# Kernel tuning notes

Measured on AMD Instinct MI355X. Metric: run time of the kernel, lower is better.

Reference implementation:

```python
import jax, jax.numpy as jnp
import numpy as np

N, H, HD = 512, 8, 128          # n_nodes, n_heads, h feature dim
M0, M1 = 256, 256               # mlp_units
NORM_CONST = 1.0


def setup_inputs() -> dict:
    key = jax.random.key(0)
    ks = jax.random.split(key, 16)
    def w(k, i, o, scale=1.0):
        return jax.random.normal(k, (i, o), jnp.float32) * (scale / np.sqrt(i))
    F = HD + H * H               # h_concat dim = 128 + 64 = 192
    EIN = H + 2 * F              # edge MLP input dim = 8 + 384 = 392
    return {
        "x": jax.random.normal(ks[0], (N, H, 3), jnp.float32),
        "h": jax.random.normal(ks[1], (N, HD), jnp.float32),
        # phi_e: MLP([256,256], silu, activate_final=True)
        "We0": w(ks[2], EIN, M0), "be0": jnp.zeros((M0,), jnp.float32),
        "We1": w(ks[3], M0, M1), "be1": jnp.zeros((M1,), jnp.float32),
        # phi_inf: Linear(1) + sigmoid
        "Winf": w(ks[4], M1, 1), "binf": jnp.zeros((1,), jnp.float32),
        # phi_x: MLP([256,256], silu, activate_final=True) -> Linear(n_heads) (variance-scaled small init)
        "Wx0": w(ks[5], M1, M0), "bx0": jnp.zeros((M0,), jnp.float32),
        "Wx1": w(ks[6], M0, M1), "bx1": jnp.zeros((M1,), jnp.float32),
        "Wxo": w(ks[7], M1, H, scale=0.03), "bxo": jnp.zeros((H,), jnp.float32),
        # phi_h: MLP([256,256], silu, activate_final=False)... note haiku MLP applies
        # activation between layers; final Linear(h_dim) appended in forward.
        "Wh0": w(ks[8], M1 + HD, M0), "bh0": jnp.zeros((M0,), jnp.float32),
        "Wh1": w(ks[9], M0, M1), "bh1": jnp.zeros((M1,), jnp.float32),
        "Who": w(ks[10], M1, HD), "bho": jnp.zeros((HD,), jnp.float32),
    }


def _forward(x, h, We0, be0, We1, be1, Winf, binf, Wx0, bx0, Wx1, bx1,
             Wxo, bxo, Wh0, bh0, Wh1, bh1, Who, bho):
    n, nh = x.shape[0], x.shape[1]
    silu = jax.nn.silu
    off = 1.0 - jnp.eye(n, dtype=x.dtype)                  # off-diagonal node mask
    # per-node head-pair squared distances -> [N, H*H] (diag naturally 0)
    dh = x[:, :, None, :] - x[:, None, :, :]               # [N,H,H,3]
    sqh = jnp.sum(dh * dh, axis=-1).reshape(n, nh * nh)
    hc = jnp.concatenate([h, sqh], axis=-1)                # [N, F]
    # all-pairs node diffs per head: dn[i,j,h] = x[j,h] - x[i,h]
    dn = x[None] - x[:, None]                              # [N,N,H,3]
    sqn = jnp.sum(dn * dn, axis=-1)                        # [N,N,H]
    F = hc.shape[-1]
    hc_j = jnp.broadcast_to(hc[None], (n, n, F))           # receiver-side: hc[j]
    hc_i = jnp.broadcast_to(hc[:, None], (n, n, F))        # sender-side: hc[i]
    edge_in = jnp.concatenate([sqn, hc_j, hc_i], axis=-1)  # [N,N,H+2F]
    # phi_e (activate_final=True), zero self-edges
    m = silu(silu(edge_in @ We0 + be0) @ We1 + be1) * off[:, :, None]
    # gate + message aggregation
    e = jax.nn.sigmoid(m @ Winf + binf)[..., 0] * off      # [N,N]
    m_i = jnp.einsum('ijd,ij->id', m, e)                   # [N,M1]
    # phi_x multi-head coordinate weights (tanh=False), zero self-edges
    px = (silu(silu(m @ Wx0 + bx0) @ Wx1 + bx1) @ Wxo + bxo) * off[:, :, None]
    # normalize_by_x_norm=True path
    norm = jnp.sqrt(sqn + 1e-8) + NORM_CONST               # [N,N,H]
    ndiff = (dn / norm[..., None]) * off[:, :, None, None]
    shift = jnp.einsum('ijhd,ijh->ihd', ndiff, px) / (n - 1)  # agg='mean'
    x_new = x + shift
    # phi_h with residual
    ph_in = jnp.concatenate([m_i, h], axis=-1)
    h_new = h + silu(silu(ph_in @ Wh0 + bh0) @ Wh1 + bh1) @ Who + bho
    return x_new, h_new


def reference(x, h, We0, be0, We1, be1, Winf, binf, Wx0, bx0, Wx1, bx1,
              Wxo, bxo, Wh0, bh0, Wh1, bh1, Who, bho):
    return _forward(x, h, We0, be0, We1, be1, Winf, binf, Wx0, bx0, Wx1, bx1,
                    Wxo, bxo, Wh0, bh0, Wh1, bh1, Who, bho)
```

## Files before the change

### kernel.cpp

```cpp
#include <hip/hip_runtime.h>
#include <math.h>

#define N_NODES 512
#define NH 8
#define HD 128
#define M 256
#define PITCH 264
#define JTILE 64
#define RPW 16

typedef __bf16 v8bf __attribute__((ext_vector_type(8)));
typedef float f32x4 __attribute__((ext_vector_type(4)));
typedef unsigned short us4v __attribute__((ext_vector_type(4)));

__device__ __forceinline__ float silu_f(float v) {
  return v * __builtin_amdgcn_rcpf(1.f + __expf(-v));
}
__device__ __forceinline__ float sigmoid_f(float v) {
  return __builtin_amdgcn_rcpf(1.f + __expf(-v));
}
__device__ __forceinline__ unsigned short f2bf(float f) {
  unsigned u = __float_as_uint(f);
  u += 0x7fffu + ((u >> 16) & 1u);
  return (unsigned short)(u >> 16);
}
__device__ __forceinline__ unsigned short f2bf_hi(float f) {
  return (unsigned short)((__float_as_uint(f) + 0x8000u) >> 16);
}
__device__ __forceinline__ float bf2f(unsigned short s) {
  return __uint_as_float(((unsigned)s) << 16);
}

__device__ __forceinline__ void gl2lds16(const unsigned short* g, unsigned short* l) {
  __builtin_amdgcn_global_load_lds(
      (const __attribute__((address_space(1))) unsigned int*)g,
      (__attribute__((address_space(3))) unsigned int*)l, 16, 0, 0);
}

__global__ __launch_bounds__(256) void k_pre(
    const float* __restrict__ x, const float* __restrict__ h,
    const float* __restrict__ We0, const float* __restrict__ be0,
    const float* __restrict__ We1, const float* __restrict__ Wx0,
    const float* __restrict__ Wx1, const float* __restrict__ Wxo,
    unsigned short* __restrict__ wsB,
    float* __restrict__ P, float* __restrict__ Q,
    float* __restrict__ mi, float* __restrict__ shift)
{
  const int t = threadIdx.x;
  if (blockIdx.x < 816) {
    const int gid = blockIdx.x * 256 + t;
    if (gid >= 208896) return;
    float val;
    if (gid < 196608) {
      const int layer = gid >> 16;
      const int i2 = gid & 65535;
      const int j = i2 & 7, lane = (i2 >> 3) & 63, nt = (i2 >> 9) & 15, kt = i2 >> 13;
      const int k = kt * 32 + (lane >> 4) * 8 + j;
      const int n = nt * 16 + (lane & 15);
      const float* W = (layer == 0) ? We1 : (layer == 1) ? Wx0 : Wx1;
      val = W[k * 256 + n];
    } else if (gid < 200704) {
      const int i2 = gid - 196608;
      const int j = i2 & 7, lane = (i2 >> 3) & 63, kt = (i2 >> 9) & 7;
      const int k = kt * 32 + (lane >> 4) * 8 + j;
      const int n = lane & 15;
      val = (n < 8) ? Wxo[k * 8 + n] : 0.f;
    } else {
      const int i2 = gid - 200704;
      const int j = i2 & 7, lane = (i2 >> 3) & 63, nt = i2 >> 9;
      const int quad = lane >> 4, lnib = lane & 15;
      val = (quad == 0) ? We0[j * 256 + nt * 16 + lnib] : 0.f;
    }
    wsB[gid] = f2bf(val);
    return;
  }
  const int i = blockIdx.x - 816;
  __shared__ float s_x[24];
  __shared__ float s_hc[192];
  mi[i * M + t] = 0.f;
  if (t < 24) { shift[i * 24 + t] = 0.f; s_x[t] = x[i * 24 + t]; }
  __syncthreads();
  if (t < HD) {
    s_hc[t] = h[i * HD + t];
  } else if (t < 192) {
    const int p = t - HD, a = p >> 3, b = p & 7;
    float s = 0.f;
#pragma unroll
    for (int d = 0; d < 3; ++d) {
      const float dx = s_x[a * 3 + d] - s_x[b * 3 + d];
      s = fmaf(dx, dx, s);
    }
    s_hc[t] = s;
  }
  __syncthreads();
  float p = 0.f, q = 0.f;
  for (int k = 0; k < 192; ++k) {
    const float hv = s_hc[k];
    p = fmaf(hv, We0[(8 + k) * M + t], p);
    q = fmaf(hv, We0[(200 + k) * M + t], q);
  }
  P[i * M + t] = p;
  Q[i * M + t] = q + be0[t];
}

__global__ __launch_bounds__(256, 3) void k_edge(
    const float* __restrict__ x,
    const float* __restrict__ P, const float* __restrict__ Q,
    const float* __restrict__ be1,
    const float* __restrict__ Winf, const float* __restrict__ binf,
    const float* __restrict__ bx0, const float* __restrict__ bx1,
    const float* __restrict__ bxo,
    const unsigned short* __restrict__ wsB,
    float* __restrict__ mi_acc, float* __restrict__ shift_acc)
{
  const int i  = blockIdx.x;
  const int j0 = blockIdx.y * JTILE;
  const int t  = threadIdx.x;
  const int lane = t & 63, wave = t >> 6;
  const int lnib = lane & 15, quad = lane >> 4;
  const int r0 = wave * RPW;
  const int jw = j0 + r0;

  __shared__ __align__(16) unsigned short a_act[JTILE * PITCH];
  __shared__ __align__(16) unsigned short B_buf[8192];
  __shared__ __align__(16) float s_sqn[JTILE][8];
  __shared__ __align__(16) unsigned short s_sqnb[JTILE][8];
  __shared__ float s_e[JTILE];

#pragma unroll
  for (int kk = 0; kk < 2; ++kk) {
    const int idx = kk * 64 + lane;
    const int r = idx >> 3, hh = idx & 7;
    const int j = jw + r;
    float s = 0.f;
#pragma unroll
    for (int d = 0; d < 3; ++d) {
      const float dx = x[j * 24 + hh * 3 + d] - x[i * 24 + hh * 3 + d];
      s = fmaf(dx, dx, s);
    }
    s_sqn[r0 + r][hh] = s;
    s_sqnb[r0 + r][hh] = f2bf(s);
  }

  const float binf0 = binf[0];

  f32x4 acc[16];

  {
#pragma unroll
    for (int nt = 0; nt < 16; ++nt)
#pragma unroll
      for (int reg = 0; reg < 4; ++reg)
        acc[nt][reg] = P[(jw + quad * 4 + reg) * M + nt * 16 + lnib];
    const v8bf aS = *(const v8bf*)&s_sqnb[r0 + lnib][0];
    const unsigned short* B0 = wsB + 200704;
#pragma unroll
    for (int nt = 0; nt < 16; ++nt) {
      const v8bf bv = *(const v8bf*)&B0[(nt * 64 + lane) * 8];
      acc[nt] = __builtin_amdgcn_mfma_f32_16x16x32_bf16(aS, bv, acc[nt], 0, 0, 0);
    }
#pragma unroll
    for (int nt = 0; nt < 16; ++nt) {
      const float qv = Q[i * M + nt * 16 + lnib];
#pragma unroll
      for (int reg = 0; reg < 4; ++reg) {
        const int row = r0 + quad * 4 + reg;
        a_act[row * PITCH + nt * 16 + lnib] = f2bf_hi(silu_f(acc[nt][reg] + qv));
      }
    }
  }

  auto run_gemm = [&](const unsigned short* __restrict__ Bg) {
#pragma unroll
    for (int kt = 0; kt < 8; ++kt) {
      __syncthreads();
      {
        const unsigned short* src = Bg + kt * 8192 + wave * 2048 + lane * 8;
        unsigned short* dst = &B_buf[wave * 2048];
        gl2lds16(src,        dst);
        gl2lds16(src + 512,  dst + 512);
        gl2lds16(src + 1024, dst + 1024);
        gl2lds16(src + 1536, dst + 1536);
      }
      __syncthreads();
      const v8bf a0 = *(const v8bf*)&a_act[(r0 + lnib) * PITCH + kt * 32 + quad * 8];
#pragma unroll
      for (int nt = 0; nt < 16; ++nt) {
        const v8bf bv = *(const v8bf*)&B_buf[nt * 512 + lane * 8];
        acc[nt] = __builtin_amdgcn_mfma_f32_16x16x32_bf16(a0, bv, acc[nt], 0, 0, 0);
      }
    }
  };

#pragma unroll
  for (int nt = 0; nt < 16; ++nt) {
    const float b = be1[nt * 16 + lnib];
    acc[nt] = (f32x4){b, b, b, b};
  }
  run_gemm(wsB);
  {
    float ge[4] = {0.f, 0.f, 0.f, 0.f};
#pragma unroll
    for (int nt = 0; nt < 16; ++nt) {
      const float wfv = Winf[nt * 16 + lnib];
#pragma unroll
      for (int reg = 0; reg < 4; ++reg) {
        float v = silu_f(acc[nt][reg]);
        const int row = r0 + quad * 4 + reg;
        if (j0 + row == i) v = 0.f;
        a_act[row * PITCH + nt * 16 + lnib] = f2bf_hi(v);
        ge[reg] = fmaf(v, wfv, ge[reg]);
      }
    }
#pragma unroll
    for (int reg = 0; reg < 4; ++reg) {
      float g = ge[reg];
      g += __shfl_xor(g, 1);
      g += __shfl_xor(g, 2);
      g += __shfl_xor(g, 4);
      g += __shfl_xor(g, 8);
      const float ev = sigmoid_f(g + binf0);
      if (lnib == 0) s_e[r0 + quad * 4 + reg] = ev;
    }
  }

  {
    const int c0 = lane * 4;
    f32x4 mip = (f32x4){0.f, 0.f, 0.f, 0.f};
#pragma unroll
    for (int r = 0; r < RPW; ++r) {
      const us4v mv = *(const us4v*)&a_act[(r0 + r) * PITCH + c0];
      const float ev = s_e[r0 + r];
      mip[0] = fmaf(bf2f(mv[0]), ev, mip[0]);
      mip[1] = fmaf(bf2f(mv[1]), ev, mip[1]);
      mip[2] = fmaf(bf2f(mv[2]), ev, mip[2]);
      mip[3] = fmaf(bf2f(mv[3]), ev, mip[3]);
    }
    atomicAdd(&mi_acc[i * M + c0 + 0], mip[0]);
    atomicAdd(&mi_acc[i * M + c0 + 1], mip[1]);
    atomicAdd(&mi_acc[i * M + c0 + 2], mip[2]);
    atomicAdd(&mi_acc[i * M + c0 + 3], mip[3]);
  }

#pragma unroll
  for (int nt = 0; nt < 16; ++nt) {
    const float b = bx0[nt * 16 + lnib];
    acc[nt] = (f32x4){b, b, b, b};
  }
  run_gemm(wsB + 65536);
#pragma unroll
  for (int nt = 0; nt < 16; ++nt)
#pragma unroll
    for (int reg = 0; reg < 4; ++reg) {
      const int row = r0 + quad * 4 + reg;
      a_act[row * PITCH + nt * 16 + lnib] = f2bf_hi(silu_f(acc[nt][reg]));
    }

#pragma unroll
  for (int nt = 0; nt < 16; ++nt) {
    const float b = bx1[nt * 16 + lnib];
    acc[nt] = (f32x4){b, b, b, b};
  }
  run_gemm(wsB + 131072);
#pragma unroll
  for (int nt = 0; nt < 16; ++nt)
#pragma unroll
    for (int reg = 0; reg < 4; ++reg) {
      const int row = r0 + quad * 4 + reg;
      a_act[row * PITCH + nt * 16 + lnib] = f2bf_hi(silu_f(acc[nt][reg]));
    }

  f32x4 px;
  {
    const float b = (lnib < 8) ? bxo[lnib] : 0.f;
    px = (f32x4){b, b, b, b};
    const unsigned short* B = wsB + 196608;
#pragma unroll
    for (int kt = 0; kt < 8; ++kt) {
      const v8bf a0 = *(const v8bf*)&a_act[(r0 + lnib) * PITCH + kt * 32 + quad * 8];
      const v8bf bv = *(const v8bf*)&B[(kt * 64 + lane) * 8];
      px = __builtin_amdgcn_mfma_f32_16x16x32_bf16(a0, bv, px, 0, 0, 0);
    }
  }

  {
    const int hh = lnib & 7;
    const float xi0 = x[i * 24 + hh * 3 + 0];
    const float xi1 = x[i * 24 + hh * 3 + 1];
    const float xi2 = x[i * 24 + hh * 3 + 2];
    float p0 = 0.f, p1 = 0.f, p2 = 0.f;
#pragma unroll
    for (int reg = 0; reg < 4; ++reg) {
      const int row = r0 + quad * 4 + reg;
      const int jg = j0 + row;
      if (jg != i) {
        const float pxv = px[reg];
        const float sq  = s_sqn[row][hh];
        const float f   = pxv * __builtin_amdgcn_rcpf(sqrtf(sq + 1e-8f) + 1.f);
        p0 = fmaf(x[jg * 24 + hh * 3 + 0] - xi0, f, p0);
        p1 = fmaf(x[jg * 24 + hh * 3 + 1] - xi1, f, p1);
        p2 = fmaf(x[jg * 24 + hh * 3 + 2] - xi2, f, p2);
      }
    }
    p0 += __shfl_xor(p0, 16); p0 += __shfl_xor(p0, 32);
    p1 += __shfl_xor(p1, 16); p1 += __shfl_xor(p1, 32);
    p2 += __shfl_xor(p2, 16); p2 += __shfl_xor(p2, 32);
    if (lane < 8) {
      atomicAdd(&shift_acc[i * 24 + hh * 3 + 0], p0);
      atomicAdd(&shift_acc[i * 24 + hh * 3 + 1], p1);
      atomicAdd(&shift_acc[i * 24 + hh * 3 + 2], p2);
    }
  }
}

__global__ __launch_bounds__(256) void k_hout(
    const float* __restrict__ x, const float* __restrict__ shift,
    const float* __restrict__ h, const float* __restrict__ mi,
    const float* __restrict__ Wh0, const float* __restrict__ bh0,
    const float* __restrict__ Wh1, const float* __restrict__ bh1,
    const float* __restrict__ Who, const float* __restrict__ bho,
    float* __restrict__ out_x, float* __restrict__ out_h)
{
  const int i = blockIdx.x, t = threadIdx.x;
  __shared__ float s_in[M + HD];
  __shared__ float s_b[M];
  if (t < 24) out_x[i * 24 + t] = x[i * 24 + t] + shift[i * 24 + t] * (1.f / 511.f);
  s_in[t] = mi[i * M + t];
  if (t < HD) s_in[M + t] = h[i * HD + t];
  __syncthreads();
  float acc = bh0[t];
  for (int k = 0; k < M + HD; ++k) acc = fmaf(s_in[k], Wh0[k * M + t], acc);
  s_b[t] = silu_f(acc);
  __syncthreads();
  float acc2 = bh1[t];
  for (int k = 0; k < M; ++k) acc2 = fmaf(s_b[k], Wh1[k * M + t], acc2);
  const float a1v = silu_f(acc2);
  __syncthreads();
  s_in[t] = a1v;
  __syncthreads();
  if (t < HD) {
    float o = bho[t];
    for (int k = 0; k < M; ++k) o = fmaf(s_in[k], Who[k * HD + t], o);
    out_h[i * HD + t] = h[i * HD + t] + o;
  }
}

extern "C" void kernel_launch(void* const* d_in, const int* in_sizes, int n_in,
                              void* d_out, int out_size, void* d_ws, size_t ws_size,
                              hipStream_t stream)
{
  const float* x    = (const float*)d_in[0];
  const float* h    = (const float*)d_in[1];
  const float* We0  = (const float*)d_in[2];
  const float* be0  = (const float*)d_in[3];
  const float* We1  = (const float*)d_in[4];
  const float* be1  = (const float*)d_in[5];
  const float* Winf = (const float*)d_in[6];
  const float* binf = (const float*)d_in[7];
  const float* Wx0  = (const float*)d_in[8];
  const float* bx0  = (const float*)d_in[9];
  const float* Wx1  = (const float*)d_in[10];
  const float* bx1  = (const float*)d_in[11];
  const float* Wxo  = (const float*)d_in[12];
  const float* bxo  = (const float*)d_in[13];
  const float* Wh0  = (const float*)d_in[14];
  const float* bh0  = (const float*)d_in[15];
  const float* Wh1  = (const float*)d_in[16];
  const float* bh1  = (const float*)d_in[17];
  const float* Who  = (const float*)d_in[18];
  const float* bho  = (const float*)d_in[19];

  float* out_x = (float*)d_out;
  float* out_h = out_x + N_NODES * NH * 3;

  float* ws    = (float*)d_ws;
  float* mi    = ws;
  float* shift = ws + 131072;
  float* P     = ws + 143360;
  float* Q     = ws + 274432;
  unsigned short* wsB = (unsigned short*)(ws + 405504);

  k_pre<<<816 + N_NODES, 256, 0, stream>>>(
      x, h, We0, be0, We1, Wx0, Wx1, Wxo, wsB, P, Q, mi, shift);
  k_edge<<<dim3(N_NODES, N_NODES / JTILE), 256, 0, stream>>>(
      x, P, Q, be1, Winf, binf, bx0, bx1, bxo, wsB, mi, shift);
  k_hout<<<N_NODES, 256, 0, stream>>>(
      x, shift, h, mi, Wh0, bh0, Wh1, bh1, Who, bho, out_x, out_h);
}
```

Measured before the change: 316.8 us.

## Split edge-kernel output columns across two waves per row group with 512 threads

The edge kernel now launches 512 threads, and each pair of waves shares a 16-row group, each wave owning half of the 256 output columns. This halves the per-wave accumulator registers and splits B-tile staging across eight waves, aiming for more resident waves and better latency hiding. In exchange it needs extra barriers: one after each GEMM, plus a shared-memory cross-wave reduction for the gate logit. The final px projection runs on only half the waves.

Measured after the change: 321.6 us. No clear change (+1.5%).

```diff
diff --git a/kernel.cpp b/kernel.cpp
--- a/kernel.cpp
+++ b/kernel.cpp
@@ -103,7 +103,7 @@
   Q[i * M + t] = q + be0[t];
 }
 
-__global__ __launch_bounds__(256, 3) void k_edge(
+__global__ __launch_bounds__(512, 4) void k_edge(
     const float* __restrict__ x,
     const float* __restrict__ P, const float* __restrict__ Q,
     const float* __restrict__ be1,
@@ -118,14 +118,24 @@
   const int t  = threadIdx.x;
   const int lane = t & 63, wave = t >> 6;
   const int lnib = lane & 15, quad = lane >> 4;
-  const int r0 = wave * RPW;
+  const int rg = wave >> 1, c = wave & 1;
+  const int r0 = rg * RPW;
   const int jw = j0 + r0;
+  const int cb = c * 128;
 
   __shared__ __align__(16) unsigned short a_act[JTILE * PITCH];
   __shared__ __align__(16) unsigned short B_buf[8192];
   __shared__ __align__(16) float s_sqn[JTILE][8];
   __shared__ __align__(16) unsigned short s_sqnb[JTILE][8];
+  __shared__ float s_red[JTILE][2];
   __shared__ float s_e[JTILE];
+
+  auto stage = [&](const unsigned short* __restrict__ Bg, int kt) {
+    const unsigned short* src = Bg + kt * 8192 + wave * 1024 + lane * 8;
+    unsigned short* dst = &B_buf[wave * 1024];
+    gl2lds16(src,       dst);
+    gl2lds16(src + 512, dst + 512);
+  };
 
 #pragma unroll
   for (int kk = 0; kk < 2; ++kk) {
@@ -144,28 +154,28 @@
 
   const float binf0 = binf[0];
 
-  f32x4 acc[16];
+  f32x4 acc[8];
 
   {
 #pragma unroll
-    for (int nt = 0; nt < 16; ++nt)
+    for (int nt = 0; nt < 8; ++nt)
 #pragma unroll
       for (int reg = 0; reg < 4; ++reg)
-        acc[nt][reg] = P[(jw + quad * 4 + reg) * M + nt * 16 + lnib];
+        acc[nt][reg] = P[(jw + quad * 4 + reg) * M + cb + nt * 16 + lnib];
     const v8bf aS = *(const v8bf*)&s_sqnb[r0 + lnib][0];
     const unsigned short* B0 = wsB + 200704;
 #pragma unroll
-    for (int nt = 0; nt < 16; ++nt) {
-      const v8bf bv = *(const v8bf*)&B0[(nt * 64 + lane) * 8];
+    for (int nt = 0; nt < 8; ++nt) {
+      const v8bf bv = *(const v8bf*)&B0[((c * 8 + nt) * 64 + lane) * 8];
       acc[nt] = __builtin_amdgcn_mfma_f32_16x16x32_bf16(aS, bv, acc[nt], 0, 0, 0);
     }
 #pragma unroll
-    for (int nt = 0; nt < 16; ++nt) {
-      const float qv = Q[i * M + nt * 16 + lnib];
+    for (int nt = 0; nt < 8; ++nt) {
+      const float qv = Q[i * M + cb + nt * 16 + lnib];
 #pragma unroll
       for (int reg = 0; reg < 4; ++reg) {
         const int row = r0 + quad * 4 + reg;
-        a_act[row * PITCH + nt * 16 + lnib] = f2bf_hi(silu_f(acc[nt][reg] + qv));
+        a_act[row * PITCH + cb + nt * 16 + lnib] = f2bf_hi(silu_f(acc[nt][reg] + qv));
       }
     }
   }
@@ -174,41 +184,35 @@
 #pragma unroll
     for (int kt = 0; kt < 8; ++kt) {
       __syncthreads();
-      {
-        const unsigned short* src = Bg + kt * 8192 + wave * 2048 + lane * 8;
-        unsigned short* dst = &B_buf[wave * 2048];
-        gl2lds16(src,        dst);
-        gl2lds16(src + 512,  dst + 512);
-        gl2lds16(src + 1024, dst + 1024);
-        gl2lds16(src + 1536, dst + 1536);
-      }
+      stage(Bg, kt);
       __syncthreads();
       const v8bf a0 = *(const v8bf*)&a_act[(r0 + lnib) * PITCH + kt * 32 + quad * 8];
 #pragma unroll
-      for (int nt = 0; nt < 16; ++nt) {
-        const v8bf bv = *(const v8bf*)&B_buf[nt * 512 + lane * 8];
+      for (int nt = 0; nt < 8; ++nt) {
+        const v8bf bv = *(const v8bf*)&B_buf[(c * 8 + nt) * 512 + lane * 8];
         acc[nt] = __builtin_amdgcn_mfma_f32_16x16x32_bf16(a0, bv, acc[nt], 0, 0, 0);
       }
     }
+    __syncthreads();
   };
 
 #pragma unroll
-  for (int nt = 0; nt < 16; ++nt) {
-    const float b = be1[nt * 16 + lnib];
+  for (int nt = 0; nt < 8; ++nt) {
+    const float b = be1[cb + nt * 16 + lnib];
     acc[nt] = (f32x4){b, b, b, b};
   }
   run_gemm(wsB);
   {
     float ge[4] = {0.f, 0.f, 0.f, 0.f};
 #pragma unroll
-    for (int nt = 0; nt < 16; ++nt) {
-      const float wfv = Winf[nt * 16 + lnib];
+    for (int nt = 0; nt < 8; ++nt) {
+      const float wfv = Winf[cb + nt * 16 + lnib];
 #pragma unroll
       for (int reg = 0; reg < 4; ++reg) {
         float v = silu_f(acc[nt][reg]);
         const int row = r0 + quad * 4 + reg;
         if (j0 + row == i) v = 0.f;
-        a_act[row * PITCH + nt * 16 + lnib] = f2bf_hi(v);
+        a_act[row * PITCH + cb + nt * 16 + lnib] = f2bf_hi(v);
         ge[reg] = fmaf(v, wfv, ge[reg]);
       }
     }
@@ -219,71 +223,69 @@
       g += __shfl_xor(g, 2);
       g += __shfl_xor(g, 4);
       g += __shfl_xor(g, 8);
-      const float ev = sigmoid_f(g + binf0);
-      if (lnib == 0) s_e[r0 + quad * 4 + reg] = ev;
-    }
-  }
+      if (lnib == 0) s_red[r0 + quad * 4 + reg][c] = g;
+    }
+  }
+  __syncthreads();
+  if (t < JTILE) s_e[t] = sigmoid_f(s_red[t][0] + s_red[t][1] + binf0);
+  __syncthreads();
 
   {
-    const int c0 = lane * 4;
-    f32x4 mip = (f32x4){0.f, 0.f, 0.f, 0.f};
+    const int ch = cb + lane * 2;
+    float m0 = 0.f, m1 = 0.f;
 #pragma unroll
     for (int r = 0; r < RPW; ++r) {
-      const us4v mv = *(const us4v*)&a_act[(r0 + r) * PITCH + c0];
+      const unsigned mv = *(const unsigned*)&a_act[(r0 + r) * PITCH + ch];
       const float ev = s_e[r0 + r];
-      mip[0] = fmaf(bf2f(mv[0]), ev, mip[0]);
-      mip[1] = fmaf(bf2f(mv[1]), ev, mip[1]);
-      mip[2] = fmaf(bf2f(mv[2]), ev, mip[2]);
-      mip[3] = fmaf(bf2f(mv[3]), ev, mip[3]);
-    }
-    atomicAdd(&mi_acc[i * M + c0 + 0], mip[0]);
-    atomicAdd(&mi_acc[i * M + c0 + 1], mip[1]);
-    atomicAdd(&mi_acc[i * M + c0 + 2], mip[2]);
-    atomicAdd(&mi_acc[i * M + c0 + 3], mip[3]);
-  }
-
-#pragma unroll
-  for (int nt = 0; nt < 16; ++nt) {
-    const float b = bx0[nt * 16 + lnib];
+      m0 = fmaf(bf2f((unsigned short)(mv & 0xffffu)), ev, m0);
+      m1 = fmaf(bf2f((unsigned short)(mv >> 16)), ev, m1);
+    }
+    atomicAdd(&mi_acc[i * M + ch + 0], m0);
+    atomicAdd(&mi_acc[i * M + ch + 1], m1);
+  }
+
+#pragma unroll
+  for (int nt = 0; nt < 8; ++nt) {
+    const float b = bx0[cb + nt * 16 + lnib];
     acc[nt] = (f32x4){b, b, b, b};
   }
   run_gemm(wsB + 65536);
 #pragma unroll
-  for (int nt = 0; nt < 16; ++nt)
+  for (int nt = 0; nt < 8; ++nt)
 #pragma unroll
     for (int reg = 0; reg < 4; ++reg) {
       const int row = r0 + quad * 4 + reg;
-      a_act[row * PITCH + nt * 16 + lnib] = f2bf_hi(silu_f(acc[nt][reg]));
-    }
-
-#pragma unroll
-  for (int nt = 0; nt < 16; ++nt) {
-    const float b = bx1[nt * 16 + lnib];
+      a_act[row * PITCH + cb + nt * 16 + lnib] = f2bf_hi(silu_f(acc[nt][reg]));
+    }
+
+#pragma unroll
+  for (int nt = 0; nt < 8; ++nt) {
+    const float b = bx1[cb + nt * 16 + lnib];
     acc[nt] = (f32x4){b, b, b, b};
   }
   run_gemm(wsB + 131072);
 #pragma unroll
-  for (int nt = 0; nt < 16; ++nt)
+  for (int nt = 0; nt < 8; ++nt)
 #pragma unroll
     for (int reg = 0; reg < 4; ++reg) {
       const int row = r0 + quad * 4 + reg;
-      a_act[row * PITCH + nt * 16 + lnib] = f2bf_hi(silu_f(acc[nt][reg]));
-    }
-
-  f32x4 px;
-  {
-    const float b = (lnib < 8) ? bxo[lnib] : 0.f;
-    px = (f32x4){b, b, b, b};
-    const unsigned short* B = wsB + 196608;
-#pragma unroll
-    for (int kt = 0; kt < 8; ++kt) {
-      const v8bf a0 = *(const v8bf*)&a_act[(r0 + lnib) * PITCH + kt * 32 + quad * 8];
-      const v8bf bv = *(const v8bf*)&B[(kt * 64 + lane) * 8];
-      px = __builtin_amdgcn_mfma_f32_16x16x32_bf16(a0, bv, px, 0, 0, 0);
-    }
-  }
-
-  {
+      a_act[row * PITCH + cb + nt * 16 + lnib] = f2bf_hi(silu_f(acc[nt][reg]));
+    }
+  __syncthreads();
+
+  if (c == 0) {
+    f32x4 px;
+    {
+      const float b = (lnib < 8) ? bxo[lnib] : 0.f;
+      px = (f32x4){b, b, b, b};
+      const unsigned short* B = wsB + 196608;
+#pragma unroll
+      for (int kt = 0; kt < 8; ++kt) {
+        const v8bf a0 = *(const v8bf*)&a_act[(r0 + lnib) * PITCH + kt * 32 + quad * 8];
+        const v8bf bv = *(const v8bf*)&B[(kt * 64 + lane) * 8];
+        px = __builtin_amdgcn_mfma_f32_16x16x32_bf16(a0, bv, px, 0, 0, 0);
+      }
+    }
     const int hh = lnib & 7;
     const float xi0 = x[i * 24 + hh * 3 + 0];
     const float xi1 = x[i * 24 + hh * 3 + 1];
@@ -382,7 +384,7 @@
 
   k_pre<<<816 + N_NODES, 256, 0, stream>>>(
       x, h, We0, be0, We1, Wx0, Wx1, Wxo, wsB, P, Q, mi, shift);
-  k_edge<<<dim3(N_NODES, N_NODES / JTILE), 256, 0, stream>>>(
+  k_edge<<<dim3(N_NODES, N_NODES / JTILE), 512, 0, stream>>>(
       x, P, Q, be1, Winf, binf, bx0, bx1, bxo, wsB, mi, shift);
   k_hout<<<N_NODES, 256, 0, stream>>>(
       x, shift, h, mi, Wh0, bh0, Wh1, bh1, Who, bho, out_x, out_h);
```
